# Kernel optimization log

Hardware: AMD Instinct MI355X
Metric: run time of the kernel (lower is better)

## Reference

```python
import jax, jax.numpy as jnp
import numpy as np

N, E = 50000, 800000
IN_CH, HID, MSG_HID, L = 128, 256, 128, 10
EPS = 1e-5


def _xavier(key, shape):
    fan_in, fan_out = shape[-2], shape[-1]
    lim = np.sqrt(6.0 / (fan_in + fan_out))
    return jax.random.uniform(key, shape, jnp.float32, -lim, lim)


def setup_inputs() -> dict:
    key = jax.random.key(0)
    ks = jax.random.split(key, 10)
    x = jax.random.normal(ks[0], (N, IN_CH), jnp.float32)
    edge_index = jax.random.randint(ks[1], (2, E), 0, N, jnp.int32)
    Win = _xavier(ks[2], (IN_CH, HID))
    bin_ = jnp.zeros((HID,), jnp.float32)
    # per-layer stacked params [L, ...]
    W1 = _xavier(ks[3], (L, HID, MSG_HID))
    b1 = jnp.zeros((L, MSG_HID), jnp.float32)
    W2 = _xavier(ks[4], (L, MSG_HID, HID))
    b2 = jnp.zeros((L, HID), jnp.float32)
    U1 = _xavier(ks[5], (L, HID, HID))
    c1 = jnp.zeros((L, HID), jnp.float32)
    U2 = _xavier(ks[6], (L, HID, HID))
    c2 = jnp.zeros((L, HID), jnp.float32)
    ln_g = jnp.ones((L, HID), jnp.float32)
    ln_b = jnp.zeros((L, HID), jnp.float32)
    beta = 0.01 * jax.random.normal(ks[7], (L + 1,), jnp.float32)
    return {"x": x, "edge_index": edge_index, "Win": Win, "bin_": bin_,
            "W1": W1, "b1": b1, "W2": W2, "b2": b2,
            "U1": U1, "c1": c1, "U2": U2, "c2": c2,
            "ln_g": ln_g, "ln_b": ln_b, "beta": beta}


def reference(x, edge_index, Win, bin_, W1, b1, W2, b2, U1, c1, U2, c2, ln_g, ln_b, beta):
    n = x.shape[0]
    self_loop = jnp.arange(n, dtype=edge_index.dtype)
    src = jnp.concatenate([edge_index[0], self_loop])  # x_j (source)
    dst = jnp.concatenate([edge_index[1], self_loop])  # aggregate at target i
    counts = jax.ops.segment_sum(jnp.ones_like(dst, dtype=x.dtype), dst, num_segments=n)
    counts = counts[:, None]  # >=1 thanks to self loops

    z0 = x @ Win + bin_  # input_lin, use_activation=False

    def layer(z, p):
        w1, bb1, w2, bb2, u1, cc1, u2, cc2, g, b_ = p
        msg = jax.nn.relu(z[src] @ w1 + bb1) @ w2 + bb2       # [E+N, HID]
        m = jax.ops.segment_sum(msg, dst, num_segments=n) / counts
        h = z + m
        out = jax.nn.relu(h @ u1 + cc1) @ u2 + cc2
        mu = out.mean(-1, keepdims=True)
        var = out.var(-1, keepdims=True)
        out = (out - mu) * jax.lax.rsqrt(var + EPS) * g + b_
        return out, out

    _, zs = jax.lax.scan(layer, z0, (W1, b1, W2, b2, U1, c1, U2, c2, ln_g, ln_b))
    zs_all = jnp.concatenate([z0[None], zs], axis=0)  # [L+1, N, HID]
    betas = jax.nn.softmax(beta)
    return jnp.einsum('l,lnh->nh', betas, zs_all)
```

## Files before the change

### kernel.cpp

```cpp
#include <hip/hip_runtime.h>
#include <stdint.h>

typedef __attribute__((ext_vector_type(4))) float f32x4;
typedef __attribute__((ext_vector_type(8))) short bf16x8;

#define HIDC 256
#define MSGC 128
#define NLAYER 10

__device__ __forceinline__ ushort f2bf(float f) {
  union { float f; uint32_t u; } a; a.f = f;
  uint32_t u = a.u;
  return (ushort)((u + 0x7fffu + ((u >> 16) & 1u)) >> 16);
}
__device__ __forceinline__ float bf2f(ushort h) {
  union { float f; uint32_t u; } a; a.u = ((uint32_t)h) << 16;
  return a.f;
}

__global__ __launch_bounds__(256, 4) void gemm_w1(
    const ushort* __restrict__ A, const ushort* __restrict__ B,
    const float* __restrict__ bias, ushort* __restrict__ C, int M) {
  __shared__ ushort lA[128 * 64];
  __shared__ ushort lB[128 * 64];
  const int tid = threadIdx.x;
  const int m0 = blockIdx.x * 128;
  const int lane = tid & 63;
  const int w = tid >> 6;
  const int wm = (w >> 1) * 64;
  const int wn = (w & 1) * 64;
  const int rr = tid >> 3;
  const int cc = tid & 7;
  f32x4 acc[4][4] = {};

#pragma unroll
  for (int s = 0; s < 4; ++s) {
    const int k0 = s * 64;
#pragma unroll
    for (int p = 0; p < 4; ++p) {
      const int row = p * 32 + rr;
      const int gm = m0 + row;
      bf16x8 av = {0, 0, 0, 0, 0, 0, 0, 0};
      if (gm < M) av = *(const bf16x8*)(A + (size_t)gm * 256 + k0 + cc * 8);
      const uint32_t off = (uint32_t)((row * 128 + cc * 16) ^ ((row & 7) << 4));
      *(bf16x8*)((char*)lA + off) = av;
    }
#pragma unroll
    for (int p = 0; p < 4; ++p) {
      const int row = p * 32 + rr;
      bf16x8 bv = *(const bf16x8*)(B + (size_t)row * 256 + k0 + cc * 8);
      const uint32_t off = (uint32_t)((row * 128 + cc * 16) ^ ((row & 7) << 4));
      *(bf16x8*)((char*)lB + off) = bv;
    }
    __syncthreads();
#pragma unroll
    for (int kk = 0; kk < 2; ++kk) {
      bf16x8 ah[4];
#pragma unroll
      for (int i = 0; i < 4; ++i) {
        const int arow = wm + i * 16 + (lane & 15);
        const uint32_t ao =
            (uint32_t)((arow * 128 + kk * 64 + ((lane >> 4) * 16)) ^ ((arow & 7) << 4));
        ah[i] = *(const bf16x8*)((const char*)lA + ao);
      }
#pragma unroll
      for (int j = 0; j < 4; ++j) {
        const int brow = wn + j * 16 + (lane & 15);
        const uint32_t bo =
            (uint32_t)((brow * 128 + kk * 64 + ((lane >> 4) * 16)) ^ ((brow & 7) << 4));
        const bf16x8 bv = *(const bf16x8*)((const char*)lB + bo);
#pragma unroll
        for (int i = 0; i < 4; ++i)
          acc[i][j] = __builtin_amdgcn_mfma_f32_16x16x32_bf16(ah[i], bv, acc[i][j], 0, 0, 0);
      }
    }
    __syncthreads();
  }
  float bi[4];
#pragma unroll
  for (int j = 0; j < 4; ++j) bi[j] = bias[wn + j * 16 + (lane & 15)];
#pragma unroll
  for (int i = 0; i < 4; ++i) {
    const int gm0 = m0 + wm + i * 16 + ((lane >> 4) << 2);
#pragma unroll
    for (int r = 0; r < 4; ++r) {
      const int gm = gm0 + r;
      if (gm < M) {
        const size_t base = (size_t)gm * 128 + wn + (lane & 15);
#pragma unroll
        for (int j = 0; j < 4; ++j)
          C[base + j * 16] = f2bf(fmaxf(acc[i][j][r] + bi[j], 0.f));
      }
    }
  }
}

template <int RELU, int ADDZ, int LN>
__global__ __launch_bounds__(512, 4) void gemm_big(
    const ushort* __restrict__ A, const ushort* __restrict__ B,
    const float* __restrict__ bias, const ushort* __restrict__ Z,
    ushort* __restrict__ C, const float* __restrict__ g,
    const float* __restrict__ b_, int M, int K) {
  __shared__ ushort lA[128 * 64];
  __shared__ ushort lB[256 * 64];
  __shared__ float sstat[2][4][128];
  const int tid = threadIdx.x;
  const int m0 = blockIdx.x * 128;
  const int lane = tid & 63;
  const int w = tid >> 6;
  const int wm = (w >> 2) * 64;
  const int wn = (w & 3) * 64;
  const int rr = tid >> 3;
  const int cc = tid & 7;
  f32x4 acc[4][4] = {};

  const int nsteps = K >> 6;
  for (int s = 0; s < nsteps; ++s) {
    const int k0 = s * 64;
#pragma unroll
    for (int p = 0; p < 2; ++p) {
      const int row = p * 64 + rr;
      const int gm = m0 + row;
      bf16x8 av = {0, 0, 0, 0, 0, 0, 0, 0};
      if (gm < M) av = *(const bf16x8*)(A + (size_t)gm * K + k0 + cc * 8);
      const uint32_t off = (uint32_t)((row * 128 + cc * 16) ^ ((row & 7) << 4));
      *(bf16x8*)((char*)lA + off) = av;
    }
#pragma unroll
    for (int p = 0; p < 4; ++p) {
      const int row = p * 64 + rr;
      bf16x8 bv = *(const bf16x8*)(B + (size_t)row * K + k0 + cc * 8);
      const uint32_t off = (uint32_t)((row * 128 + cc * 16) ^ ((row & 7) << 4));
      *(bf16x8*)((char*)lB + off) = bv;
    }
    __syncthreads();
#pragma unroll
    for (int kk = 0; kk < 2; ++kk) {
      bf16x8 ah[4];
#pragma unroll
      for (int i = 0; i < 4; ++i) {
        const int arow = wm + i * 16 + (lane & 15);
        const uint32_t ao =
            (uint32_t)((arow * 128 + kk * 64 + ((lane >> 4) * 16)) ^ ((arow & 7) << 4));
        ah[i] = *(const bf16x8*)((const char*)lA + ao);
      }
#pragma unroll
      for (int j = 0; j < 4; ++j) {
        const int brow = wn + j * 16 + (lane & 15);
        const uint32_t bo =
            (uint32_t)((brow * 128 + kk * 64 + ((lane >> 4) * 16)) ^ ((brow & 7) << 4));
        const bf16x8 bv = *(const bf16x8*)((const char*)lB + bo);
#pragma unroll
        for (int i = 0; i < 4; ++i)
          acc[i][j] = __builtin_amdgcn_mfma_f32_16x16x32_bf16(ah[i], bv, acc[i][j], 0, 0, 0);
      }
    }
    __syncthreads();
  }

  float bi[4];
#pragma unroll
  for (int j = 0; j < 4; ++j) bi[j] = bias[wn + j * 16 + (lane & 15)];

  if (LN) {
    float gv[4], bv[4];
#pragma unroll
    for (int j = 0; j < 4; ++j) {
      gv[j] = g[wn + j * 16 + (lane & 15)];
      bv[j] = b_[wn + j * 16 + (lane & 15)];
    }
#pragma unroll
    for (int i = 0; i < 4; ++i) {
#pragma unroll
      for (int r = 0; r < 4; ++r) {
        float s1 = 0.f, s2 = 0.f;
#pragma unroll
        for (int j = 0; j < 4; ++j) {
          float v = acc[i][j][r] + bi[j];
          acc[i][j][r] = v;
          s1 += v;
          s2 += v * v;
        }
#pragma unroll
        for (int d = 1; d < 16; d <<= 1) {
          s1 += __shfl_xor(s1, d);
          s2 += __shfl_xor(s2, d);
        }
        if ((lane & 15) == 0) {
          const int rl = wm + i * 16 + ((lane >> 4) << 2) + r;
          sstat[0][w & 3][rl] = s1;
          sstat[1][w & 3][rl] = s2;
        }
      }
    }
    __syncthreads();
#pragma unroll
    for (int i = 0; i < 4; ++i) {
#pragma unroll
      for (int r = 0; r < 4; ++r) {
        const int rl = wm + i * 16 + ((lane >> 4) << 2) + r;
        const float s1 = sstat[0][0][rl] + sstat[0][1][rl] + sstat[0][2][rl] + sstat[0][3][rl];
        const float s2 = sstat[1][0][rl] + sstat[1][1][rl] + sstat[1][2][rl] + sstat[1][3][rl];
        const float mu = s1 * (1.f / 256.f);
        const float var = s2 * (1.f / 256.f) - mu * mu;
        const float rs = rsqrtf(var + 1e-5f);
        const int gm = m0 + rl;
        if (gm < M) {
          const size_t base = (size_t)gm * 256 + wn + (lane & 15);
#pragma unroll
          for (int j = 0; j < 4; ++j)
            C[base + j * 16] = f2bf((acc[i][j][r] - mu) * rs * gv[j] + bv[j]);
        }
      }
    }
  } else {
#pragma unroll
    for (int i = 0; i < 4; ++i) {
      const int gm0 = m0 + wm + i * 16 + ((lane >> 4) << 2);
#pragma unroll
      for (int r = 0; r < 4; ++r) {
        const int gm = gm0 + r;
        if (gm < M) {
          const size_t base = (size_t)gm * 256 + wn + (lane & 15);
#pragma unroll
          for (int j = 0; j < 4; ++j) {
            float v = acc[i][j][r] + bi[j];
            if (ADDZ) v += bf2f(Z[base + j * 16]);
            if (RELU) v = fmaxf(v, 0.f);
            C[base + j * 16] = f2bf(v);
          }
        }
      }
    }
  }
}

template <int WRITE>
__global__ __launch_bounds__(256) void fold_kernel(
    const ushort* __restrict__ zbase, size_t ZS, const float* __restrict__ betas,
    int l0, int P, float* __restrict__ outp, int total8) {
  const int i = blockIdx.x * 256 + threadIdx.x;
  if (i >= total8) return;
  float a[8] = {};
  for (int k = 0; k < P; ++k) {
    const float bl = betas[l0 + k];
    const uint4 u = ((const uint4*)(zbase + k * ZS))[i];
    const uint32_t ww[4] = {u.x, u.y, u.z, u.w};
#pragma unroll
    for (int q = 0; q < 4; ++q) {
      union { uint32_t u; float f; } lo, hi;
      lo.u = ww[q] << 16;
      hi.u = ww[q] & 0xffff0000u;
      a[2 * q] += bl * lo.f;
      a[2 * q + 1] += bl * hi.f;
    }
  }
  f32x4 o0 = {a[0], a[1], a[2], a[3]};
  f32x4 o1 = {a[4], a[5], a[6], a[7]};
  if (WRITE) {
    ((f32x4*)outp)[(size_t)i * 2] = o0;
    ((f32x4*)outp)[(size_t)i * 2 + 1] = o1;
  } else {
    f32x4 p0 = ((f32x4*)outp)[(size_t)i * 2];
    f32x4 p1 = ((f32x4*)outp)[(size_t)i * 2 + 1];
    ((f32x4*)outp)[(size_t)i * 2] = p0 + o0;
    ((f32x4*)outp)[(size_t)i * 2 + 1] = p1 + o1;
  }
}

__global__ void count_kernel(const int* __restrict__ dstv, int* __restrict__ deg, int E) {
  int i = blockIdx.x * 256 + threadIdx.x;
  if (i < E) atomicAdd(&deg[dstv[i]], 1);
}

__global__ void scanA_kernel(const int* __restrict__ deg, int* __restrict__ excl,
                             int* __restrict__ bsum, int n) {
  __shared__ int sm[256];
  const int i = blockIdx.x * 256 + threadIdx.x;
  const int v = (i < n) ? deg[i] : 0;
  sm[threadIdx.x] = v;
  __syncthreads();
  for (int off = 1; off < 256; off <<= 1) {
    int t = (threadIdx.x >= off) ? sm[threadIdx.x - off] : 0;
    __syncthreads();
    sm[threadIdx.x] += t;
    __syncthreads();
  }
  if (i < n) excl[i] = sm[threadIdx.x] - v;
  if (threadIdx.x == 255) bsum[blockIdx.x] = sm[255];
}

__global__ void scanB_kernel(const int* __restrict__ bsum, int* __restrict__ boff, int nb) {
  __shared__ int sm[256];
  const int v = (threadIdx.x < nb) ? bsum[threadIdx.x] : 0;
  sm[threadIdx.x] = v;
  __syncthreads();
  for (int off = 1; off < 256; off <<= 1) {
    int t = (threadIdx.x >= off) ? sm[threadIdx.x - off] : 0;
    __syncthreads();
    sm[threadIdx.x] += t;
    __syncthreads();
  }
  if (threadIdx.x < nb) boff[threadIdx.x] = sm[threadIdx.x] - v;
}

__global__ void scanC_kernel(const int* __restrict__ deg, const int* __restrict__ excl,
                             const int* __restrict__ boff, int* __restrict__ rowptr,
                             int* __restrict__ fillptr, float* __restrict__ invc,
                             int n, int E) {
  const int i = blockIdx.x * 256 + threadIdx.x;
  if (i < n) {
    const int r = excl[i] + boff[blockIdx.x];
    rowptr[i] = r;
    fillptr[i] = r;
    invc[i] = 1.0f / (float)(deg[i] + 1);
  }
  if (i == 0) rowptr[n] = E;
}

__global__ void fill_kernel(const int* __restrict__ srcv, const int* __restrict__ dstv,
                            int* __restrict__ fillptr, int* __restrict__ colv, int E) {
  int i = blockIdx.x * 256 + threadIdx.x;
  if (i < E) {
    int p = atomicAdd(&fillptr[dstv[i]], 1);
    colv[p] = srcv[i];
  }
}

__global__ __launch_bounds__(256) void agg128_kernel(
    const uint32_t* __restrict__ T, const int* __restrict__ rowptr,
    const int* __restrict__ colv, const float* __restrict__ invc,
    uint32_t* __restrict__ sout, int n) {
  const int node = blockIdx.x * 4 + (threadIdx.x >> 6);
  if (node >= n) return;
  const int lane = threadIdx.x & 63;
  auto up0 = [](uint32_t u) {
    union { uint32_t u; float f; } a; a.u = u << 16; return a.f;
  };
  auto up1 = [](uint32_t u) {
    union { uint32_t u; float f; } a; a.u = u & 0xffff0000u; return a.f;
  };
  const uint32_t self = T[(size_t)node * 64 + lane];
  float a0 = up0(self), a1 = up1(self);
  float b0 = 0.f, b1 = 0.f, c0 = 0.f, c1 = 0.f, d0 = 0.f, d1 = 0.f;
  const int s = rowptr[node];
  const int e = rowptr[node + 1];
  int i = s;
  for (; i + 3 < e; i += 4) {
    const int s0 = colv[i], s1 = colv[i + 1], s2 = colv[i + 2], s3 = colv[i + 3];
    const uint32_t u0 = T[(size_t)s0 * 64 + lane];
    const uint32_t u1 = T[(size_t)s1 * 64 + lane];
    const uint32_t u2 = T[(size_t)s2 * 64 + lane];
    const uint32_t u3 = T[(size_t)s3 * 64 + lane];
    a0 += up0(u0); a1 += up1(u0);
    b0 += up0(u1); b1 += up1(u1);
    c0 += up0(u2); c1 += up1(u2);
    d0 += up0(u3); d1 += up1(u3);
  }
  for (; i < e; ++i) {
    const uint32_t u0 = T[(size_t)colv[i] * 64 + lane];
    a0 += up0(u0); a1 += up1(u0);
  }
  const float ic = invc[node];
  const float r0 = (a0 + b0 + c0 + d0) * ic;
  const float r1 = (a1 + b1 + c1 + d1) * ic;
  sout[(size_t)node * 64 + lane] = (uint32_t)f2bf(r0) | ((uint32_t)f2bf(r1) << 16);
}

__global__ void beta_kernel(const float* __restrict__ beta, float* __restrict__ betas) {
  if (threadIdx.x == 0) {
    float mx = beta[0];
    for (int i = 1; i < NLAYER + 1; ++i) mx = fmaxf(mx, beta[i]);
    float e[NLAYER + 1];
    float s = 0.f;
    for (int i = 0; i < NLAYER + 1; ++i) {
      e[i] = expf(beta[i] - mx);
      s += e[i];
    }
    const float inv = 1.f / s;
    for (int i = 0; i < NLAYER + 1; ++i) betas[i] = e[i] * inv;
  }
}

__global__ void wconv_kernel(const float* __restrict__ W, ushort* __restrict__ Wt,
                             int K, int Nn) {
  const size_t matoff = (size_t)blockIdx.z * K * Nn;
  const int o = blockIdx.x * 256 + threadIdx.x;
  if (o >= K * Nn) return;
  const int nn = o / K;
  const int kk = o - nn * K;
  Wt[matoff + o] = f2bf(W[matoff + (size_t)kk * Nn + nn]);
}

__global__ void xcast_kernel(const float* __restrict__ x, ushort* __restrict__ xb, int n8) {
  const int i = blockIdx.x * 256 + threadIdx.x;
  if (i >= n8) return;
  const f32x4 v0 = ((const f32x4*)x)[(size_t)i * 2];
  const f32x4 v1 = ((const f32x4*)x)[(size_t)i * 2 + 1];
  bf16x8 o;
#pragma unroll
  for (int q = 0; q < 4; ++q) {
    o[q] = (short)f2bf(v0[q]);
    o[q + 4] = (short)f2bf(v1[q]);
  }
  *(bf16x8*)(xb + (size_t)i * 8) = o;
}

extern "C" void kernel_launch(void* const* d_in, const int* in_sizes, int n_in,
                              void* d_out, int out_size, void* d_ws, size_t ws_size,
                              hipStream_t stream) {
  const float* x = (const float*)d_in[0];
  const int* eidx = (const int*)d_in[1];
  const float* Win = (const float*)d_in[2];
  const float* bin_ = (const float*)d_in[3];
  const float* W1 = (const float*)d_in[4];
  const float* b1 = (const float*)d_in[5];
  const float* W2 = (const float*)d_in[6];
  const float* b2 = (const float*)d_in[7];
  const float* U1 = (const float*)d_in[8];
  const float* c1 = (const float*)d_in[9];
  const float* U2 = (const float*)d_in[10];
  const float* c2 = (const float*)d_in[11];
  const float* ln_g = (const float*)d_in[12];
  const float* ln_b = (const float*)d_in[13];
  const float* beta = (const float*)d_in[14];
  float* outp = (float*)d_out;

  const int Nn = in_sizes[0] / 128;
  const int E = in_sizes[1] / 2;
  const int* srcv = eidx;
  const int* dstv = eidx + E;

  char* p = (char*)d_ws;
  auto alloc = [&](size_t bytes) {
    char* r = p;
    p += (bytes + 255) & ~(size_t)255;
    return r;
  };
  ushort* hbuf = (ushort*)alloc((size_t)Nn * HIDC * 2);
  ushort* TSO = (ushort*)alloc((size_t)Nn * HIDC * 2);
  ushort* xbf = (ushort*)alloc((size_t)Nn * 128 * 2);
  ushort* WinT = (ushort*)alloc(128 * 256 * 2);
  ushort* W1T = (ushort*)alloc((size_t)NLAYER * 256 * 128 * 2);
  ushort* W2T = (ushort*)alloc((size_t)NLAYER * 128 * 256 * 2);
  ushort* U1T = (ushort*)alloc((size_t)NLAYER * 256 * 256 * 2);
  ushort* U2T = (ushort*)alloc((size_t)NLAYER * 256 * 256 * 2);
  int* deg = (int*)alloc((size_t)Nn * 4);
  int* rowptr = (int*)alloc((size_t)(Nn + 1) * 4);
  int* fillptr = (int*)alloc((size_t)Nn * 4);
  float* invc = (float*)alloc((size_t)Nn * 4);
  int* colv = (int*)alloc((size_t)E * 4);
  int* excl = (int*)alloc((size_t)Nn * 4);
  int* bsum = (int*)alloc(256 * 4);
  int* boff = (int*)alloc(256 * 4);
  float* betas = (float*)alloc(64);

  const size_t ZS = (size_t)Nn * HIDC;
  const size_t slotB = ZS * 2;
  const size_t used = (size_t)(p - (char*)d_ws);
  int G = 2;
  if (ws_size > used + 4096) {
    size_t fit = (ws_size - used - 4096) / (slotB + 256);
    G = (int)(fit < 2 ? 2 : (fit > NLAYER + 1 ? NLAYER + 1 : fit));
  }
  ushort* zbase = (ushort*)alloc((size_t)G * slotB);

  ushort* T128 = TSO;
  ushort* s128 = TSO + (size_t)Nn * MSGC;
  ushort* Obuf = TSO;

  const int nscan = (Nn + 255) / 256;
  const int mb128 = (Nn + 127) / 128;
  const int nwave = (Nn + 3) / 4;
  const int total8 = (Nn * HIDC) / 8;

  hipMemsetAsync(deg, 0, (size_t)Nn * 4, stream);
  count_kernel<<<(E + 255) / 256, 256, 0, stream>>>(dstv, deg, E);
  scanA_kernel<<<nscan, 256, 0, stream>>>(deg, excl, bsum, Nn);
  scanB_kernel<<<1, 256, 0, stream>>>(bsum, boff, nscan);
  scanC_kernel<<<nscan, 256, 0, stream>>>(deg, excl, boff, rowptr, fillptr, invc, Nn, E);
  fill_kernel<<<(E + 255) / 256, 256, 0, stream>>>(srcv, dstv, fillptr, colv, E);
  beta_kernel<<<1, 64, 0, stream>>>(beta, betas);
  xcast_kernel<<<(Nn * 16 + 255) / 256, 256, 0, stream>>>(x, xbf, Nn * 16);
  wconv_kernel<<<dim3(128, 1, 1), 256, 0, stream>>>(Win, WinT, 128, 256);
  wconv_kernel<<<dim3(128, 1, NLAYER), 256, 0, stream>>>(W1, W1T, 256, 128);
  wconv_kernel<<<dim3(128, 1, NLAYER), 256, 0, stream>>>(W2, W2T, 128, 256);
  wconv_kernel<<<dim3(256, 1, NLAYER), 256, 0, stream>>>(U1, U1T, 256, 256);
  wconv_kernel<<<dim3(256, 1, NLAYER), 256, 0, stream>>>(U2, U2T, 256, 256);

  int pend = 0, l0 = 0;
  bool first = true;
  auto flush = [&]() {
    if (pend > 0) {
      if (first)
        fold_kernel<1><<<(total8 + 255) / 256, 256, 0, stream>>>(zbase, ZS, betas, l0,
                                                                 pend, outp, total8);
      else
        fold_kernel<0><<<(total8 + 255) / 256, 256, 0, stream>>>(zbase, ZS, betas, l0,
                                                                 pend, outp, total8);
      first = false;
      l0 += pend;
      pend = 0;
    }
  };

  ushort* zcur = zbase;
  gemm_big<0, 0, 0><<<mb128, 512, 0, stream>>>(xbf, WinT, bin_, nullptr, zcur, nullptr,
                                               nullptr, Nn, 128);
  pend = 1;

  for (int l = 0; l < NLAYER; ++l) {
    gemm_w1<<<mb128, 256, 0, stream>>>(zcur, W1T + (size_t)l * 256 * 128, b1 + l * 128,
                                       T128, Nn);
    agg128_kernel<<<nwave, 256, 0, stream>>>((const uint32_t*)T128, rowptr, colv, invc,
                                             (uint32_t*)s128, Nn);
    gemm_big<0, 1, 0><<<mb128, 512, 0, stream>>>(s128, W2T + (size_t)l * 128 * 256,
                                                 b2 + l * 256, zcur, hbuf, nullptr,
                                                 nullptr, Nn, 128);
    gemm_big<1, 0, 0><<<mb128, 512, 0, stream>>>(hbuf, U1T + (size_t)l * 256 * 256,
                                                 c1 + l * 256, nullptr, Obuf, nullptr,
                                                 nullptr, Nn, 256);
    if (pend == G) flush();
    ushort* znext = zbase + (size_t)pend * slotB / 2;
    gemm_big<0, 0, 1><<<mb128, 512, 0, stream>>>(Obuf, U2T + (size_t)l * 256 * 256,
                                                 c2 + l * 256, nullptr, znext,
                                                 ln_g + l * 256, ln_b + l * 256, Nn, 256);
    zcur = znext;
    pend++;
  }
  flush();
}
```

Before: 1.464 ms.

## Vectorize aggregation gathers, batch preprocessing atomics, add dedicated input GEMM kernel

The aggregation kernel now assigns 16 lanes per node, each gathering a 16-byte uint4 of 8 bf16 values, where before 64 lanes each loaded 4 bytes. This reduces gather instruction count and packs more nodes per block. The count and fill kernels each process 4 edges per thread, and the U1/U2 weight conversions are merged into one launch. A specialized gemm_win kernel with K=128 and a full 256-wide B tile replaces the generic gemm_big for the input projection. Risks include higher register pressure in aggregation and a possibly less tuned new GEMM.

```diff
diff --git a/kernel.cpp b/kernel.cpp
--- a/kernel.cpp
+++ b/kernel.cpp
@@ -269,8 +269,10 @@
 }
 
 __global__ void count_kernel(const int* __restrict__ dstv, int* __restrict__ deg, int E) {
-  int i = blockIdx.x * 256 + threadIdx.x;
-  if (i < E) atomicAdd(&deg[dstv[i]], 1);
+  const int i = (blockIdx.x * 256 + threadIdx.x) * 4;
+#pragma unroll
+  for (int k = 0; k < 4; ++k)
+    if (i + k < E) atomicAdd(&deg[dstv[i + k]], 1);
 }
 
 __global__ void scanA_kernel(const int* __restrict__ deg, int* __restrict__ excl,
@@ -320,51 +322,60 @@
 
 __global__ void fill_kernel(const int* __restrict__ srcv, const int* __restrict__ dstv,
                             int* __restrict__ fillptr, int* __restrict__ colv, int E) {
-  int i = blockIdx.x * 256 + threadIdx.x;
-  if (i < E) {
-    int p = atomicAdd(&fillptr[dstv[i]], 1);
-    colv[p] = srcv[i];
-  }
+  const int i = (blockIdx.x * 256 + threadIdx.x) * 4;
+#pragma unroll
+  for (int k = 0; k < 4; ++k)
+    if (i + k < E) {
+      int p = atomicAdd(&fillptr[dstv[i + k]], 1);
+      colv[p] = srcv[i + k];
+    }
 }
 
 __global__ __launch_bounds__(256) void agg128_kernel(
-    const uint32_t* __restrict__ T, const int* __restrict__ rowptr,
+    const ushort* __restrict__ T, const int* __restrict__ rowptr,
     const int* __restrict__ colv, const float* __restrict__ invc,
-    uint32_t* __restrict__ sout, int n) {
-  const int node = blockIdx.x * 4 + (threadIdx.x >> 6);
+    ushort* __restrict__ sout, int n) {
+  const int node = blockIdx.x * 16 + (threadIdx.x >> 4);
   if (node >= n) return;
-  const int lane = threadIdx.x & 63;
-  auto up0 = [](uint32_t u) {
-    union { uint32_t u; float f; } a; a.u = u << 16; return a.f;
+  const int q = threadIdx.x & 15;
+  const uint4* Tv = (const uint4*)T;
+  float a[8] = {}, b[8] = {}, c[8] = {}, d[8] = {};
+  auto addu = [](float* acc, uint4 u) {
+    const uint32_t ww[4] = {u.x, u.y, u.z, u.w};
+#pragma unroll
+    for (int k = 0; k < 4; ++k) {
+      union { uint32_t u; float f; } lo, hi;
+      lo.u = ww[k] << 16;
+      hi.u = ww[k] & 0xffff0000u;
+      acc[2 * k] += lo.f;
+      acc[2 * k + 1] += hi.f;
+    }
   };
-  auto up1 = [](uint32_t u) {
-    union { uint32_t u; float f; } a; a.u = u & 0xffff0000u; return a.f;
-  };
-  const uint32_t self = T[(size_t)node * 64 + lane];
-  float a0 = up0(self), a1 = up1(self);
-  float b0 = 0.f, b1 = 0.f, c0 = 0.f, c1 = 0.f, d0 = 0.f, d1 = 0.f;
+  addu(a, Tv[(size_t)node * 16 + q]);
   const int s = rowptr[node];
   const int e = rowptr[node + 1];
   int i = s;
   for (; i + 3 < e; i += 4) {
-    const int s0 = colv[i], s1 = colv[i + 1], s2 = colv[i + 2], s3 = colv[i + 3];
-    const uint32_t u0 = T[(size_t)s0 * 64 + lane];
-    const uint32_t u1 = T[(size_t)s1 * 64 + lane];
-    const uint32_t u2 = T[(size_t)s2 * 64 + lane];
-    const uint32_t u3 = T[(size_t)s3 * 64 + lane];
-    a0 += up0(u0); a1 += up1(u0);
-    b0 += up0(u1); b1 += up1(u1);
-    c0 += up0(u2); c1 += up1(u2);
-    d0 += up0(u3); d1 += up1(u3);
-  }
-  for (; i < e; ++i) {
-    const uint32_t u0 = T[(size_t)colv[i] * 64 + lane];
-    a0 += up0(u0); a1 += up1(u0);
-  }
+    const uint4 u0 = Tv[(size_t)colv[i] * 16 + q];
+    const uint4 u1 = Tv[(size_t)colv[i + 1] * 16 + q];
+    const uint4 u2 = Tv[(size_t)colv[i + 2] * 16 + q];
+    const uint4 u3 = Tv[(size_t)colv[i + 3] * 16 + q];
+    addu(a, u0);
+    addu(b, u1);
+    addu(c, u2);
+    addu(d, u3);
+  }
+  for (; i < e; ++i) addu(a, Tv[(size_t)colv[i] * 16 + q]);
   const float ic = invc[node];
-  const float r0 = (a0 + b0 + c0 + d0) * ic;
-  const float r1 = (a1 + b1 + c1 + d1) * ic;
-  sout[(size_t)node * 64 + lane] = (uint32_t)f2bf(r0) | ((uint32_t)f2bf(r1) << 16);
+  uint4 o;
+  uint32_t* ow = (uint32_t*)&o;
+#pragma unroll
+  for (int k = 0; k < 4; ++k) {
+    const float r0 = (a[2 * k] + b[2 * k] + c[2 * k] + d[2 * k]) * ic;
+    const float r1 = (a[2 * k + 1] + b[2 * k + 1] + c[2 * k + 1] + d[2 * k + 1]) * ic;
+    ow[k] = (uint32_t)f2bf(r0) | ((uint32_t)f2bf(r1) << 16);
+  }
+  ((uint4*)sout)[(size_t)node * 16 + q] = o;
 }
 
 __global__ void beta_kernel(const float* __restrict__ beta, float* __restrict__ betas) {
@@ -392,6 +403,18 @@
   Wt[matoff + o] = f2bf(W[matoff + (size_t)kk * Nn + nn]);
 }
 
+__global__ void wconvU_kernel(const float* __restrict__ U1, const float* __restrict__ U2,
+                              ushort* __restrict__ U1T, ushort* __restrict__ U2T) {
+  const int li = blockIdx.z;
+  const float* W = (li < NLAYER) ? U1 : U2;
+  ushort* Wt = (li < NLAYER) ? U1T : U2T;
+  const size_t matoff = (size_t)(li % NLAYER) * 256 * 256;
+  const int o = blockIdx.x * 256 + threadIdx.x;
+  const int nn = o >> 8;
+  const int kk = o & 255;
+  Wt[matoff + o] = f2bf(W[matoff + (size_t)kk * 256 + nn]);
+}
+
 __global__ void xcast_kernel(const float* __restrict__ x, ushort* __restrict__ xb, int n8) {
   const int i = blockIdx.x * 256 + threadIdx.x;
   if (i >= n8) return;
@@ -404,6 +427,84 @@
     o[q + 4] = (short)f2bf(v1[q]);
   }
   *(bf16x8*)(xb + (size_t)i * 8) = o;
+}
+
+__global__ __launch_bounds__(512, 4) void gemm_win(
+    const ushort* __restrict__ A, const ushort* __restrict__ B,
+    const float* __restrict__ bias, ushort* __restrict__ C, int M) {
+  __shared__ ushort lA[128 * 64];
+  __shared__ ushort lB[256 * 64];
+  const int tid = threadIdx.x;
+  const int m0 = blockIdx.x * 128;
+  const int lane = tid & 63;
+  const int w = tid >> 6;
+  const int wm = (w >> 2) * 64;
+  const int wn = (w & 3) * 64;
+  const int rr = tid >> 3;
+  const int cc = tid & 7;
+  f32x4 acc[4][4] = {};
+  const int K = 128;
+
+#pragma unroll
+  for (int s = 0; s < 2; ++s) {
+    const int k0 = s * 64;
+#pragma unroll
+    for (int p = 0; p < 2; ++p) {
+      const int row = p * 64 + rr;
+      const int gm = m0 + row;
+      bf16x8 av = {0, 0, 0, 0, 0, 0, 0, 0};
+      if (gm < M) av = *(const bf16x8*)(A + (size_t)gm * K + k0 + cc * 8);
+      const uint32_t off = (uint32_t)((row * 128 + cc * 16) ^ ((row & 7) << 4));
+      *(bf16x8*)((char*)lA + off) = av;
+    }
+#pragma unroll
+    for (int p = 0; p < 4; ++p) {
+      const int row = p * 64 + rr;
+      bf16x8 bv = *(const bf16x8*)(B + (size_t)row * K + k0 + cc * 8);
+      const uint32_t off = (uint32_t)((row * 128 + cc * 16) ^ ((row & 7) << 4));
+      *(bf16x8*)((char*)lB + off) = bv;
+    }
+    __syncthreads();
+#pragma unroll
+    for (int kk = 0; kk < 2; ++kk) {
+      bf16x8 ah[4];
+#pragma unroll
+      for (int i = 0; i < 4; ++i) {
+        const int arow = wm + i * 16 + (lane & 15);
+        const uint32_t ao =
+            (uint32_t)((arow * 128 + kk * 64 + ((lane >> 4) * 16)) ^ ((arow & 7) << 4));
+        ah[i] = *(const bf16x8*)((const char*)lA + ao);
+      }
+#pragma unroll
+      for (int j = 0; j < 4; ++j) {
+        const int brow = wn + j * 16 + (lane & 15);
+        const uint32_t bo =
+            (uint32_t)((brow * 128 + kk * 64 + ((lane >> 4) * 16)) ^ ((brow & 7) << 4));
+        const bf16x8 bv = *(const bf16x8*)((const char*)lB + bo);
+#pragma unroll
+        for (int i = 0; i < 4; ++i)
+          acc[i][j] = __builtin_amdgcn_mfma_f32_16x16x32_bf16(ah[i], bv, acc[i][j], 0, 0, 0);
+      }
+    }
+    __syncthreads();
+  }
+  float bi[4];
+#pragma unroll
+  for (int j = 0; j < 4; ++j) bi[j] = bias[wn + j * 16 + (lane & 15)];
+#pragma unroll
+  for (int i = 0; i < 4; ++i) {
+    const int gm0 = m0 + wm + i * 16 + ((lane >> 4) << 2);
+#pragma unroll
+    for (int r = 0; r < 4; ++r) {
+      const int gm = gm0 + r;
+      if (gm < M) {
+        const size_t base = (size_t)gm * 256 + wn + (lane & 15);
+#pragma unroll
+        for (int j = 0; j < 4; ++j)
+          C[base + j * 16] = f2bf(acc[i][j][r] + bi[j]);
+      }
+    }
+  }
 }
 
 extern "C" void kernel_launch(void* const* d_in, const int* in_sizes, int n_in,
@@ -471,22 +572,21 @@
 
   const int nscan = (Nn + 255) / 256;
   const int mb128 = (Nn + 127) / 128;
-  const int nwave = (Nn + 3) / 4;
+  const int nagg = (Nn + 15) / 16;
   const int total8 = (Nn * HIDC) / 8;
 
   hipMemsetAsync(deg, 0, (size_t)Nn * 4, stream);
-  count_kernel<<<(E + 255) / 256, 256, 0, stream>>>(dstv, deg, E);
+  count_kernel<<<(E + 1023) / 1024, 256, 0, stream>>>(dstv, deg, E);
   scanA_kernel<<<nscan, 256, 0, stream>>>(deg, excl, bsum, Nn);
   scanB_kernel<<<1, 256, 0, stream>>>(bsum, boff, nscan);
   scanC_kernel<<<nscan, 256, 0, stream>>>(deg, excl, boff, rowptr, fillptr, invc, Nn, E);
-  fill_kernel<<<(E + 255) / 256, 256, 0, stream>>>(srcv, dstv, fillptr, colv, E);
+  fill_kernel<<<(E + 1023) / 1024, 256, 0, stream>>>(srcv, dstv, fillptr, colv, E);
   beta_kernel<<<1, 64, 0, stream>>>(beta, betas);
   xcast_kernel<<<(Nn * 16 + 255) / 256, 256, 0, stream>>>(x, xbf, Nn * 16);
   wconv_kernel<<<dim3(128, 1, 1), 256, 0, stream>>>(Win, WinT, 128, 256);
   wconv_kernel<<<dim3(128, 1, NLAYER), 256, 0, stream>>>(W1, W1T, 256, 128);
   wconv_kernel<<<dim3(128, 1, NLAYER), 256, 0, stream>>>(W2, W2T, 128, 256);
-  wconv_kernel<<<dim3(256, 1, NLAYER), 256, 0, stream>>>(U1, U1T, 256, 256);
-  wconv_kernel<<<dim3(256, 1, NLAYER), 256, 0, stream>>>(U2, U2T, 256, 256);
+  wconvU_kernel<<<dim3(256, 1, 2 * NLAYER), 256, 0, stream>>>(U1, U2, U1T, U2T);
 
   int pend = 0, l0 = 0;
   bool first = true;
@@ -505,15 +605,13 @@
   };
 
   ushort* zcur = zbase;
-  gemm_big<0, 0, 0><<<mb128, 512, 0, stream>>>(xbf, WinT, bin_, nullptr, zcur, nullptr,
-                                               nullptr, Nn, 128);
+  gemm_win<<<mb128, 512, 0, stream>>>(xbf, WinT, bin_, zcur, Nn);
   pend = 1;
 
   for (int l = 0; l < NLAYER; ++l) {
     gemm_w1<<<mb128, 256, 0, stream>>>(zcur, W1T + (size_t)l * 256 * 128, b1 + l * 128,
                                        T128, Nn);
-    agg128_kernel<<<nwave, 256, 0, stream>>>((const uint32_t*)T128, rowptr, colv, invc,
-                                             (uint32_t*)s128, Nn);
+    agg128_kernel<<<nagg, 256, 0, stream>>>(T128, rowptr, colv, invc, s128, Nn);
     gemm_big<0, 1, 0><<<mb128, 512, 0, stream>>>(s128, W2T + (size_t)l * 128 * 256,
                                                  b2 + l * 256, zcur, hbuf, nullptr,
                                                  nullptr, Nn, 128);
@@ -521,7 +619,7 @@
                                                  c1 + l * 256, nullptr, Obuf, nullptr,
                                                  nullptr, Nn, 256);
     if (pend == G) flush();
-    ushort* znext = zbase + (size_t)pend * slotB / 2;
+    ushort* znext = zbase + (size_t)pend * ZS;
     gemm_big<0, 0, 1><<<mb128, 512, 0, stream>>>(Obuf, U2T + (size_t)l * 256 * 256,
                                                  c2 + l * 256, nullptr, znext,
                                                  ln_g + l * 256, ln_b + l * 256, Nn, 256);
```

Result: no change. 1.440 ms (-1.6%).
